# Optimization experiments

Hardware: AMD Instinct MI355X
Metric: run time of the kernel (lower is better)

The kernel has to match this reference:

```python
import jax, jax.numpy as jnp
import numpy as np

HID, HEADS = 2048, 16
Q_LORA, KV_LORA = 1536, 512
NOPE, ROPE, VD = 128, 64, 128
N_EXP, TOPK, MOE_I, SH_I = 8, 2, 1408, 2816
EPS, RSF = 1e-6, 1.0
ROPE_BASE = 10000.0


def _rms(x, w):
    return x * jax.lax.rsqrt(jnp.mean(jnp.square(x), -1, keepdims=True) + EPS) * w


def _rope(x, pos):
    # neox-style rotary on last dim; x: [T, H, d], pos: [T]
    d = x.shape[-1]
    inv = 1.0 / (ROPE_BASE ** (jnp.arange(0, d, 2, dtype=jnp.float32) / d))
    ang = pos.astype(jnp.float32)[:, None] * inv  # [T, d/2]
    cos, sin = jnp.cos(ang)[:, None, :], jnp.sin(ang)[:, None, :]
    x1, x2 = x[..., : d // 2], x[..., d // 2:]
    return jnp.concatenate([x1 * cos - x2 * sin, x2 * cos + x1 * sin], -1)


def setup_inputs() -> dict:
    key = jax.random.key(0)
    ks = jax.random.split(key, 16)
    T, s, f = 1024, 0.02, jnp.float32
    return {
        'positions': jnp.arange(T, dtype=jnp.int32),
        'hidden_states': jax.random.normal(ks[0], (T, HID), f),
        'residual': jax.random.normal(ks[1], (T, HID), f),
        'w_in_ln': jnp.ones((HID,), f),
        'w_post_ln': jnp.ones((HID,), f),
        'w_q_ln': jnp.ones((Q_LORA,), f),
        'w_kv_ln': jnp.ones((KV_LORA,), f),
        'w_qkv_a': jax.random.normal(ks[2], (HID, Q_LORA + KV_LORA + ROPE), f) * s,
        'w_q_b': jax.random.normal(ks[3], (Q_LORA, HEADS * (NOPE + ROPE)), f) * s,
        'w_kv_b': jax.random.normal(ks[4], (KV_LORA, HEADS * (NOPE + VD)), f) * s,
        'w_o': jax.random.normal(ks[5], (HEADS * VD, HID), f) * s,
        'gate_w': jax.random.normal(ks[6], (HID, N_EXP), f) * s,
        'we_gate': jax.random.normal(ks[7], (N_EXP, HID, MOE_I), f) * s,
        'we_up': jax.random.normal(ks[8], (N_EXP, HID, MOE_I), f) * s,
        'we_down': jax.random.normal(ks[9], (N_EXP, MOE_I, HID), f) * s,
        'ws_gate': jax.random.normal(ks[10], (HID, SH_I), f) * s,
        'ws_up': jax.random.normal(ks[11], (HID, SH_I), f) * s,
        'ws_down': jax.random.normal(ks[12], (SH_I, HID), f) * s,
    }


def reference(positions, hidden_states, residual, w_in_ln, w_post_ln, w_q_ln, w_kv_ln,
              w_qkv_a, w_q_b, w_kv_b, w_o, gate_w, we_gate, we_up, we_down,
              ws_gate, ws_up, ws_down):
    T = hidden_states.shape[0]
    # fused_add_rms_norm: residual <- x + residual; x <- rmsnorm(residual)
    residual = hidden_states + residual
    h = _rms(residual, w_in_ln)
    # fused qkv_a projection and split
    qkv = h @ w_qkv_a  # [T, q_lora + kv_lora + rope]
    q_c = _rms(qkv[:, :Q_LORA], w_q_ln)
    kv_c = _rms(qkv[:, Q_LORA:Q_LORA + KV_LORA], w_kv_ln)
    k_pe = qkv[:, Q_LORA + KV_LORA:][:, None, :]  # [T, 1, rope]
    # MLA up-projections
    q = (q_c @ w_q_b).reshape(T, HEADS, NOPE + ROPE)
    q_nope, q_pe = q[..., :NOPE], q[..., NOPE:]
    kv = (kv_c @ w_kv_b).reshape(T, HEADS, NOPE + VD)
    k_nope, v = kv[..., :NOPE], kv[..., NOPE:]
    q_pe = _rope(q_pe, positions)
    k_pe = _rope(k_pe, positions)
    q = jnp.concatenate([q_nope, q_pe], -1)  # [T, H, nope+rope]
    k = jnp.concatenate([k_nope, jnp.broadcast_to(k_pe, (T, HEADS, ROPE))], -1)
    scores = jnp.einsum('qhd,khd->hqk', q, k) * (NOPE + ROPE) ** -0.5
    causal = jnp.tril(jnp.ones((T, T), bool))
    scores = jnp.where(causal, scores, jnp.finfo(scores.dtype).min)
    p = jax.nn.softmax(scores, -1)
    attn_out = jnp.einsum('hqk,khd->qhd', p, v).reshape(T, HEADS * VD) @ w_o
    # post-attention fused add + norm
    residual = residual + attn_out
    h = _rms(residual, w_post_ln)
    # MoE gate: softmax scores, top-k, renormalized combine weights
    probs = jax.nn.softmax(h @ gate_w, -1)
    tw, ti = jax.lax.top_k(probs, TOPK)
    tw = tw / jnp.sum(tw, -1, keepdims=True)
    comb = jnp.sum(jax.nn.one_hot(ti, N_EXP, dtype=h.dtype) * tw[..., None], 1)  # [T, E]
    # routed experts (dense grouped-GEMM reference, SwiGLU)
    g = jnp.einsum('th,ehi->eti', h, we_gate)
    u = jnp.einsum('th,ehi->eti', h, we_up)
    y = jnp.einsum('eti,eih->eth', jax.nn.silu(g) * u, we_down)
    routed = jnp.einsum('te,eth->th', comb, y) * RSF
    # shared experts
    shared = (jax.nn.silu(h @ ws_gate) * (h @ ws_up)) @ ws_down
    return routed + shared, residual
```

## Files before the change

kernel.cpp:

```cpp
#include <hip/hip_runtime.h>
#include <hip/hip_bf16.h>

typedef unsigned short u16;
typedef __attribute__((ext_vector_type(8))) short bf16x8;
typedef __attribute__((ext_vector_type(4))) float f32x4;
typedef __attribute__((ext_vector_type(8))) unsigned short u16x8;
typedef __attribute__((ext_vector_type(4))) unsigned short u16x4;

#define T_TOK 1024
#define HID 2048
#define HEADS 16
#define Q_LORA 1536
#define KV_LORA 512
#define NOPE 128
#define ROPED 64
#define VD 128
#define N_EXP 8
#define MOE_I 1408
#define SH_I 2816
#define QKV_N 2112
#define QKV_LD 2176
#define QD 192
#define KVD 256
#define EPSF 1e-6f
#define NEG_BIG (-3.4e38f)

__device__ __forceinline__ u16 f2bf(float f) {
  union { float f; unsigned u; } x; x.f = f;
  unsigned r = x.u + 0x7fffu + ((x.u >> 16) & 1u);
  return (u16)(r >> 16);
}
__device__ __forceinline__ float bf2f(u16 h) {
  union { unsigned u; float f; } x; x.u = ((unsigned)h) << 16; return x.f;
}
__device__ __forceinline__ void split2(float f, u16& hi, u16& lo) {
  hi = f2bf(f);
  lo = f2bf(f - bf2f(hi));
}

__device__ __forceinline__ void gload16(const u16* g, const u16* l) {
  __builtin_amdgcn_global_load_lds(
      (const __attribute__((address_space(1))) void*)g,
      (__attribute__((address_space(3))) void*)l, 16, 0, 0);
}

__device__ __forceinline__ float block_sum(float v, float* s) {
  #pragma unroll
  for (int o = 32; o > 0; o >>= 1) v += __shfl_down(v, o, 64);
  int w = threadIdx.x >> 6, lane = threadIdx.x & 63;
  __syncthreads();
  if (lane == 0) s[w] = v;
  __syncthreads();
  float r = s[0];
  for (int i = 1; i < 4; ++i) r += s[i];
  return r;
}
__device__ __forceinline__ float block_max(float v, float* s) {
  #pragma unroll
  for (int o = 32; o > 0; o >>= 1) v = fmaxf(v, __shfl_down(v, o, 64));
  int w = threadIdx.x >> 6, lane = threadIdx.x & 63;
  __syncthreads();
  if (lane == 0) s[w] = v;
  __syncthreads();
  float r = s[0];
  for (int i = 1; i < 4; ++i) r = fmaxf(r, s[i]);
  return r;
}

__global__ __launch_bounds__(256) void gemm_bf16(
    const u16* __restrict__ A, long asz, int lda,
    const u16* __restrict__ B, long bsz, int ldb,
    float* __restrict__ C, u16* __restrict__ Cb, long csz, int ldc,
    const float* __restrict__ Cadd, const u16* __restrict__ CaddB, int ldcadd,
    int K, float alpha, int causal, int mode,
    float* __restrict__ pbuf, int ksplit, int stot, int soff,
    const int* __restrict__ gidx, const int* __restrict__ gcnt) {
  const int bm = blockIdx.y << 7, bn = blockIdx.x << 7;
  const int zz = blockIdx.z;
  const int z = (ksplit > 1) ? (zz / ksplit) : zz;
  const int s = (ksplit > 1) ? (zz % ksplit) : 0;
  if (gcnt && bm >= gcnt[z]) return;
  A += (long)z * asz; B += (long)z * bsz;
  if (C) C += (long)z * csz;
  if (Cb) Cb += (long)z * csz;
  if (Cadd && !pbuf) Cadd += (long)z * csz;
  if (CaddB) CaddB += (long)z * csz;
  const int tid = threadIdx.x, lane = tid & 63, wid = tid >> 6;

  if (causal && bn >= bm + 128) return;

  __shared__ alignas(16) u16 As[128 * 32];
  __shared__ alignas(16) u16 Bs[128 * 32];

  const int wr = wid >> 1, wc = wid & 1;
  f32x4 acc[4][4];
  #pragma unroll
  for (int m = 0; m < 4; ++m)
    #pragma unroll
    for (int n = 0; n < 4; ++n) acc[m][n] = f32x4{0.f, 0.f, 0.f, 0.f};

  const int srow = (wid << 5) + (lane >> 2);
  const int scol = (lane & 3) << 3;
  const int arow = (wr << 6) + (lane & 15);
  const int brow = (wc << 6) + (lane & 15);
  const int koff = (lane >> 4) << 3;

  long ga0, ga1;
  {
    int r0 = srow, r1 = srow + 16;
    if (gidx) {
      const int* tk = gidx + (long)z * T_TOK;
      ga0 = (long)tk[bm + r0]; ga1 = (long)tk[bm + r1];
    } else {
      ga0 = (long)(bm + r0); ga1 = (long)(bm + r1);
    }
  }

  const int kseg = K / ksplit;
  const int kbeg = s * kseg, kend = kbeg + kseg;

  for (int k0 = kbeg; k0 < kend; k0 += 32) {
    gload16(A + ga0 * lda + k0 + scol, &As[(wid << 10)]);
    gload16(A + ga1 * lda + k0 + scol, &As[(wid << 10) + 512]);
    gload16(B + (long)(bn + srow) * ldb + k0 + scol, &Bs[(wid << 10)]);
    gload16(B + (long)(bn + srow + 16) * ldb + k0 + scol, &Bs[(wid << 10) + 512]);
    __syncthreads();
    bf16x8 a[4], b[4];
    #pragma unroll
    for (int m = 0; m < 4; ++m) a[m] = *(const bf16x8*)&As[((arow + (m << 4)) << 5) + koff];
    #pragma unroll
    for (int n = 0; n < 4; ++n) b[n] = *(const bf16x8*)&Bs[((brow + (n << 4)) << 5) + koff];
    #pragma unroll
    for (int m = 0; m < 4; ++m)
      #pragma unroll
      for (int n = 0; n < 4; ++n)
        acc[m][n] = __builtin_amdgcn_mfma_f32_16x16x32_bf16(a[m], b[n], acc[m][n], 0, 0, 0);
    __syncthreads();
  }

  const int rbase = bm + (wr << 6) + ((lane >> 4) << 2);
  const int cbase = bn + (wc << 6) + (lane & 15);

  if (pbuf) {
    long pstride = (long)(gridDim.y << 7) * ldc;
    float* pp = pbuf + ((long)z * stot + soff + s) * pstride;
    #pragma unroll
    for (int m = 0; m < 4; ++m)
      #pragma unroll
      for (int j = 0; j < 4; ++j) {
        int r = rbase + (m << 4) + j;
        #pragma unroll
        for (int n = 0; n < 4; ++n) {
          int cc = cbase + (n << 4);
          pp[(long)r * ldc + cc] = acc[m][n][j];
        }
      }
    return;
  }

  #pragma unroll
  for (int m = 0; m < 4; ++m) {
    #pragma unroll
    for (int j = 0; j < 4; ++j) {
      int r = rbase + (m << 4) + j;
      #pragma unroll
      for (int n = 0; n < 4; ++n) {
        int cc = cbase + (n << 4);
        float v = acc[m][n][j] * alpha;
        if (mode == 0) {
          if (Cadd) v += Cadd[(long)r * ldcadd + cc];
          if (causal && cc > r) v = NEG_BIG;
          C[(long)r * ldc + cc] = v;
        } else if (mode == 1) {
          float gg = Cadd[(long)r * ldcadd + cc];
          float sgv = gg / (1.f + expf(-gg));
          Cb[(long)r * ldc + cc] = f2bf(sgv * v);
        } else if (mode == 2) {
          Cb[(long)r * ldc + cc] = f2bf(v);
        } else {
          float gg = bf2f(CaddB[(long)r * ldcadd + cc]);
          float sgv = gg / (1.f + expf(-gg));
          Cb[(long)r * ldc + cc] = f2bf(sgv * v);
        }
      }
    }
  }
}

__global__ __launch_bounds__(256) void reduce_sk(
    const float* __restrict__ pbuf, long pstride, int S,
    float* __restrict__ C, u16* __restrict__ Cb, long csz, int ldc, int Nc,
    const float* __restrict__ Cadd, long caddsz, int ldcadd,
    float alpha, int mode) {
  const int z = blockIdx.y;
  const float* pz = pbuf + (long)z * S * pstride;
  long idx = ((long)blockIdx.x * 256 + threadIdx.x) * 8;
  long r = idx / Nc; int c = (int)(idx - r * Nc);
  float a[8] = {0.f, 0.f, 0.f, 0.f, 0.f, 0.f, 0.f, 0.f};
  for (int s = 0; s < S; ++s) {
    const float* pp = pz + (long)s * pstride + idx;
    float4 x = *(const float4*)pp;
    float4 y = *(const float4*)(pp + 4);
    a[0] += x.x; a[1] += x.y; a[2] += x.z; a[3] += x.w;
    a[4] += y.x; a[5] += y.y; a[6] += y.z; a[7] += y.w;
  }
  long ob = (long)z * csz + r * ldc + c;
  if (mode == 0) {
    #pragma unroll
    for (int k = 0; k < 8; ++k) {
      float v = a[k] * alpha;
      if (Cadd) v += Cadd[(long)z * caddsz + r * ldcadd + c + k];
      C[ob + k] = v;
    }
  } else {
    u16x8 o;
    #pragma unroll
    for (int k = 0; k < 8; ++k) {
      float gg = Cadd[(long)z * caddsz + r * ldcadd + c + k];
      float sgv = gg / (1.f + expf(-gg));
      o[k] = f2bf(sgv * a[k] * alpha);
    }
    *(u16x8*)&Cb[ob] = o;
  }
}

__global__ __launch_bounds__(256) void transpose_f32_bf16(
    const float* __restrict__ src, long sbs, int ld_src, int Cvalid,
    u16* __restrict__ dst, long dbs, int ld_dst) {
  __shared__ float tile[64][65];
  src += (long)blockIdx.z * sbs; dst += (long)blockIdx.z * dbs;
  const int c0 = blockIdx.x << 6, r0 = blockIdx.y << 6;
  const int tid = threadIdx.x;
  const int tc = (tid & 15) << 2, tr0 = tid >> 4;
  const bool valid = c0 < Cvalid;
  #pragma unroll
  for (int i = 0; i < 4; ++i) {
    int r = tr0 + (i << 4);
    float4 v;
    if (valid) v = *(const float4*)&src[(long)(r0 + r) * ld_src + c0 + tc];
    else { v.x = 0.f; v.y = 0.f; v.z = 0.f; v.w = 0.f; }
    tile[r][tc] = v.x; tile[r][tc + 1] = v.y; tile[r][tc + 2] = v.z; tile[r][tc + 3] = v.w;
  }
  __syncthreads();
  const int oc = tid >> 2, seg = tid & 3;
  u16x8 o0, o1;
  #pragma unroll
  for (int k = 0; k < 8; ++k) o0[k] = f2bf(tile[(seg << 4) + k][oc]);
  #pragma unroll
  for (int k = 0; k < 8; ++k) o1[k] = f2bf(tile[(seg << 4) + 8 + k][oc]);
  u16* dp = &dst[(long)(c0 + oc) * ld_dst + r0 + (seg << 4)];
  *(u16x8*)dp = o0;
  *(u16x8*)(dp + 8) = o1;
}

__global__ __launch_bounds__(256) void transpose_split3(
    const float* __restrict__ src, long sbs, int ld_src, int Cvalid,
    u16* __restrict__ dst, long dbs, int Kp) {
  __shared__ float tile[64][65];
  src += (long)blockIdx.z * sbs; dst += (long)blockIdx.z * dbs;
  const int c0 = blockIdx.x << 6, r0 = blockIdx.y << 6;
  const int tid = threadIdx.x;
  const int tc = (tid & 15) << 2, tr0 = tid >> 4;
  const bool valid = c0 < Cvalid;
  #pragma unroll
  for (int i = 0; i < 4; ++i) {
    int r = tr0 + (i << 4);
    float4 v;
    if (valid) v = *(const float4*)&src[(long)(r0 + r) * ld_src + c0 + tc];
    else { v.x = 0.f; v.y = 0.f; v.z = 0.f; v.w = 0.f; }
    tile[r][tc] = v.x; tile[r][tc + 1] = v.y; tile[r][tc + 2] = v.z; tile[r][tc + 3] = v.w;
  }
  __syncthreads();
  const int oc = tid >> 2, seg = tid & 3;
  u16x8 h0, h1, l0, l1;
  #pragma unroll
  for (int k = 0; k < 8; ++k) {
    u16 hi, lo; split2(tile[(seg << 4) + k][oc], hi, lo);
    h0[k] = hi; l0[k] = lo;
  }
  #pragma unroll
  for (int k = 0; k < 8; ++k) {
    u16 hi, lo; split2(tile[(seg << 4) + 8 + k][oc], hi, lo);
    h1[k] = hi; l1[k] = lo;
  }
  const int ldd = 3 * Kp;
  u16* dp = &dst[(long)(c0 + oc) * ldd + r0 + (seg << 4)];
  *(u16x8*)dp = h0;            *(u16x8*)(dp + 8) = h1;
  *(u16x8*)(dp + Kp) = h0;     *(u16x8*)(dp + Kp + 8) = h1;
  *(u16x8*)(dp + 2 * Kp) = l0; *(u16x8*)(dp + 2 * Kp + 8) = l1;
}

__global__ __launch_bounds__(256) void conv_split3_kernel(
    const float* __restrict__ src, u16* __restrict__ dst, int C, long n) {
  long stride = (long)gridDim.x * 2048;
  for (long i = ((long)blockIdx.x * 256 + threadIdx.x) * 8; i < n; i += stride) {
    long r = i / C; int c = (int)(i - r * C);
    float4 a = *(const float4*)&src[i];
    float4 b = *(const float4*)&src[i + 4];
    u16x8 hv, lv;
    u16 hi, lo;
    split2(a.x, hi, lo); hv[0] = hi; lv[0] = lo;
    split2(a.y, hi, lo); hv[1] = hi; lv[1] = lo;
    split2(a.z, hi, lo); hv[2] = hi; lv[2] = lo;
    split2(a.w, hi, lo); hv[3] = hi; lv[3] = lo;
    split2(b.x, hi, lo); hv[4] = hi; lv[4] = lo;
    split2(b.y, hi, lo); hv[5] = hi; lv[5] = lo;
    split2(b.z, hi, lo); hv[6] = hi; lv[6] = lo;
    split2(b.w, hi, lo); hv[7] = hi; lv[7] = lo;
    u16* base = dst + r * (long)(3 * C) + c;
    *(u16x8*)base = hv;
    *(u16x8*)(base + C) = lv;
    *(u16x8*)(base + 2 * C) = hv;
  }
}

__global__ __launch_bounds__(256) void add_rms_kernel(
    const float* __restrict__ hs, const float* __restrict__ res,
    const float* __restrict__ w, float* __restrict__ resid1, u16* __restrict__ h3) {
  __shared__ float sbuf[4];
  int t = blockIdx.x;
  float v[8]; float ss = 0.f;
  #pragma unroll
  for (int i = 0; i < 8; ++i) {
    int j = threadIdx.x + (i << 8);
    float x = hs[(long)t * HID + j] + res[(long)t * HID + j];
    v[i] = x; resid1[(long)t * HID + j] = x; ss += x * x;
  }
  ss = block_sum(ss, sbuf);
  float sc = rsqrtf(ss / (float)HID + EPSF);
  u16* base = h3 + (long)t * (3 * HID);
  #pragma unroll
  for (int i = 0; i < 8; ++i) {
    int j = threadIdx.x + (i << 8);
    u16 hi, lo; split2(v[i] * sc * w[j], hi, lo);
    base[j] = hi; base[HID + j] = lo; base[2 * HID + j] = hi;
  }
}

template <int NW, bool SPLIT, bool WF32>
__global__ __launch_bounds__(256) void rms_rows_kernel(
    const float* __restrict__ in, int ldin, const float* __restrict__ w,
    u16* __restrict__ outb, float* __restrict__ outf) {
  __shared__ float sbuf[4];
  int t = blockIdx.x;
  const int W = NW * 256;
  float v[NW]; float ss = 0.f;
  #pragma unroll
  for (int i = 0; i < NW; ++i) {
    int j = threadIdx.x + (i << 8);
    float x = in[(long)t * ldin + j];
    v[i] = x; ss += x * x;
  }
  ss = block_sum(ss, sbuf);
  float sc = rsqrtf(ss / (float)W + EPSF);
  #pragma unroll
  for (int i = 0; i < NW; ++i) {
    int j = threadIdx.x + (i << 8);
    float y = v[i] * sc * w[j];
    if (SPLIT) {
      u16 hi, lo; split2(y, hi, lo);
      u16* base = outb + (long)t * (3 * W);
      base[j] = hi; base[W + j] = lo; base[2 * W + j] = hi;
    } else {
      outb[(long)t * W + j] = f2bf(y);
    }
    if (WF32) outf[(long)t * W + j] = y;
  }
}

__global__ __launch_bounds__(256) void rope_kernel(
    const int* __restrict__ pos, float* __restrict__ q,
    const float* __restrict__ qkv, float* __restrict__ kpe) {
  int t = blockIdx.x;
  float fp = (float)pos[t];
  for (int item = threadIdx.x; item < 544; item += 256) {
    int i = item & 31;
    float inv = expf(-((float)i * (2.f / 64.f)) * 9.210340371976184f);
    float ang = fp * inv;
    float c = cosf(ang), s = sinf(ang);
    if (item < 512) {
      int hh = item >> 5;
      long base = (long)t * (HEADS * QD) + hh * QD + NOPE;
      float x1 = q[base + i], x2 = q[base + 32 + i];
      q[base + i] = x1 * c - x2 * s;
      q[base + 32 + i] = x2 * c + x1 * s;
    } else {
      long base = (long)t * QKV_LD + (Q_LORA + KV_LORA);
      float x1 = qkv[base + i], x2 = qkv[base + 32 + i];
      kpe[(long)t * 64 + i] = x1 * c - x2 * s;
      kpe[(long)t * 64 + 32 + i] = x2 * c + x1 * s;
    }
  }
}

__global__ __launch_bounds__(192) void build_q3_kernel(
    const float* __restrict__ qbuf, u16* __restrict__ q3) {
  int t = blockIdx.x, h = blockIdx.y, d = threadIdx.x;
  float x = qbuf[(long)t * (HEADS * QD) + h * QD + d];
  u16 hi, lo; split2(x, hi, lo);
  u16* base = q3 + ((long)h * T_TOK + t) * (3 * QD);
  base[d] = hi; base[QD + d] = lo; base[2 * QD + d] = hi;
}

__global__ __launch_bounds__(192) void build_kmat3_kernel(
    const float* __restrict__ kv, const float* __restrict__ kpe,
    u16* __restrict__ kmat3) {
  int t = blockIdx.x, h = blockIdx.y, d = threadIdx.x;
  float v = (d < NOPE) ? kv[(long)t * (HEADS * KVD) + h * KVD + d]
                       : kpe[(long)t * 64 + (d - NOPE)];
  u16 hi, lo; split2(v, hi, lo);
  u16* base = kmat3 + ((long)h * T_TOK + t) * (3 * QD);
  base[d] = hi; base[QD + d] = hi; base[2 * QD + d] = lo;
}

__global__ __launch_bounds__(256) void softmax_kernel(
    const float* __restrict__ S, u16* __restrict__ P2) {
  __shared__ float sbuf[4];
  long row = blockIdx.x;
  int r = (int)(row & (T_TOK - 1));
  const float* p = S + row * T_TOK;
  float4 v = ((const float4*)p)[threadIdx.x];
  int c0 = threadIdx.x << 2;
  if (c0 + 0 > r) v.x = NEG_BIG;
  if (c0 + 1 > r) v.y = NEG_BIG;
  if (c0 + 2 > r) v.z = NEG_BIG;
  if (c0 + 3 > r) v.w = NEG_BIG;
  float m = fmaxf(fmaxf(v.x, v.y), fmaxf(v.z, v.w));
  m = block_max(m, sbuf);
  v.x = expf(v.x - m); v.y = expf(v.y - m); v.z = expf(v.z - m); v.w = expf(v.w - m);
  float s = v.x + v.y + v.z + v.w;
  s = block_sum(s, sbuf);
  float inv = 1.f / s;
  u16x4 hv, lv;
  u16 hi, lo;
  split2(v.x * inv, hi, lo); hv[0] = hi; lv[0] = lo;
  split2(v.y * inv, hi, lo); hv[1] = hi; lv[1] = lo;
  split2(v.z * inv, hi, lo); hv[2] = hi; lv[2] = lo;
  split2(v.w * inv, hi, lo); hv[3] = hi; lv[3] = lo;
  u16* base = P2 + row * (2 * T_TOK) + (threadIdx.x << 2);
  *(u16x4*)base = hv;
  *(u16x4*)(base + T_TOK) = lv;
}

__global__ __launch_bounds__(256) void gate_topk_kernel(
    const float* __restrict__ h2, const float* __restrict__ gw,
    int* __restrict__ ti, float* __restrict__ tw) {
  __shared__ float sbuf[4];
  __shared__ float lg[N_EXP];
  int t = blockIdx.x;
  float p[N_EXP] = {0.f, 0.f, 0.f, 0.f, 0.f, 0.f, 0.f, 0.f};
  for (int j = threadIdx.x; j < HID; j += 256) {
    float x = h2[(long)t * HID + j];
    const float* gr = gw + (long)j * N_EXP;
    #pragma unroll
    for (int e = 0; e < N_EXP; ++e) p[e] += x * gr[e];
  }
  #pragma unroll
  for (int e = 0; e < N_EXP; ++e) {
    float s = block_sum(p[e], sbuf);
    if (threadIdx.x == 0) lg[e] = s;
  }
  __syncthreads();
  if (threadIdx.x == 0) {
    float m = lg[0];
    for (int e = 1; e < N_EXP; ++e) m = fmaxf(m, lg[e]);
    float pe[N_EXP]; float s = 0.f;
    for (int e = 0; e < N_EXP; ++e) { pe[e] = expf(lg[e] - m); s += pe[e]; }
    for (int e = 0; e < N_EXP; ++e) pe[e] /= s;
    int i0 = 0;
    for (int e = 1; e < N_EXP; ++e) if (pe[e] > pe[i0]) i0 = e;
    int i1 = -1;
    for (int e = 0; e < N_EXP; ++e) if (e != i0 && (i1 < 0 || pe[e] > pe[i1])) i1 = e;
    float ssum = pe[i0] + pe[i1];
    ti[2 * t] = i0; ti[2 * t + 1] = i1;
    tw[2 * t] = pe[i0] / ssum; tw[2 * t + 1] = pe[i1] / ssum;
  }
}

__global__ __launch_bounds__(64) void route_build_kernel(
    const int* __restrict__ ti, int* __restrict__ tokidx,
    int* __restrict__ pos, int* __restrict__ cnt) {
  int e = blockIdx.x;
  int lane = threadIdx.x;
  if (e >= N_EXP) {
    for (int p = lane; p < T_TOK; p += 64) tokidx[(long)e * T_TOK + p] = p;
    if (lane == 0) cnt[e] = T_TOK;
    return;
  }
  int c = 0;
  for (int base = 0; base < T_TOK; base += 64) {
    int t = base + lane;
    int e0 = ti[2 * t], e1 = ti[2 * t + 1];
    bool match = (e0 == e) || (e1 == e);
    unsigned long long mask = __ballot(match);
    int pref = __popcll(mask & ((1ull << lane) - 1ull));
    if (match) {
      int p = c + pref;
      tokidx[(long)e * T_TOK + p] = t;
      pos[2 * t + ((e0 == e) ? 0 : 1)] = p;
    }
    c += __popcll(mask);
  }
  for (int p = c + lane; p < T_TOK; p += 64) tokidx[(long)e * T_TOK + p] = 0;
  if (lane == 0) cnt[e] = c;
}

__global__ __launch_bounds__(256) void combine_out_kernel(
    const u16* __restrict__ y, const int* __restrict__ ti,
    const float* __restrict__ tw, const int* __restrict__ pos,
    float* __restrict__ out0) {
  int t = blockIdx.x;
  int j = threadIdx.x << 3;
  int e0 = ti[2 * t], e1 = ti[2 * t + 1];
  int p0 = pos[2 * t], p1 = pos[2 * t + 1];
  float w0 = tw[2 * t], w1 = tw[2 * t + 1];
  u16x8 a = *(const u16x8*)&y[((long)e0 * T_TOK + p0) * HID + j];
  u16x8 b = *(const u16x8*)&y[((long)e1 * T_TOK + p1) * HID + j];
  u16x8 c = *(const u16x8*)&y[((long)8 * T_TOK + t) * HID + j];
  u16x8 d = *(const u16x8*)&y[((long)9 * T_TOK + t) * HID + j];
  float* rp = out0 + (long)t * HID + j;
  #pragma unroll
  for (int k = 0; k < 8; ++k)
    rp[k] = w0 * bf2f(a[k]) + w1 * bf2f(b[k]) + bf2f(c[k]) + bf2f(d[k]);
}

extern "C" void kernel_launch(void* const* d_in, const int* in_sizes, int n_in,
                              void* d_out, int out_size, void* d_ws, size_t ws_size,
                              hipStream_t stream) {
  (void)in_sizes; (void)n_in; (void)out_size; (void)ws_size;
  const int*   positions = (const int*)d_in[0];
  const float* hs        = (const float*)d_in[1];
  const float* res       = (const float*)d_in[2];
  const float* w_in_ln   = (const float*)d_in[3];
  const float* w_post_ln = (const float*)d_in[4];
  const float* w_q_ln    = (const float*)d_in[5];
  const float* w_kv_ln   = (const float*)d_in[6];
  const float* w_qkv_a   = (const float*)d_in[7];
  const float* w_q_b     = (const float*)d_in[8];
  const float* w_kv_b    = (const float*)d_in[9];
  const float* w_o       = (const float*)d_in[10];
  const float* gate_w    = (const float*)d_in[11];
  const float* we_gate   = (const float*)d_in[12];
  const float* we_up     = (const float*)d_in[13];
  const float* we_down   = (const float*)d_in[14];
  const float* ws_gate   = (const float*)d_in[15];
  const float* ws_up     = (const float*)d_in[16];
  const float* ws_dn     = (const float*)d_in[17];

  float* out0   = (float*)d_out;
  float* resid2 = out0 + (long)T_TOK * HID;

  char* Wb = (char*)d_ws;
  size_t off = 0;
  #define CARVE(name, type, bytes) type* name = (type*)(Wb + off); off += (((size_t)(bytes) + 255) & ~(size_t)255)

  CARVE(wqkvaT3, u16, (size_t)QKV_LD * 3 * HID * 2);
  CARVE(wqbT3,   u16, (size_t)(HEADS * QD) * 3 * Q_LORA * 2);
  CARVE(wkvbT3,  u16, (size_t)(HEADS * KVD) * 3 * KV_LORA * 2);
  CARVE(woT3,    u16, (size_t)HID * 3 * HID * 2);

  size_t pool = off;
  CARVE(resid1, float, (size_t)T_TOK * HID * 4);
  CARVE(h3,     u16,   (size_t)T_TOK * 3 * HID * 2);
  CARVE(qkv,    float, (size_t)T_TOK * QKV_LD * 4);
  CARVE(qc3,    u16,   (size_t)T_TOK * 3 * Q_LORA * 2);
  CARVE(kvc3,   u16,   (size_t)T_TOK * 3 * KV_LORA * 2);
  CARVE(qbuf,   float, (size_t)T_TOK * HEADS * QD * 4);
  CARVE(q3,     u16,   (size_t)HEADS * T_TOK * 3 * QD * 2);
  CARVE(kvbuf,  float, (size_t)T_TOK * HEADS * KVD * 4);
  CARVE(kpe,    float, (size_t)T_TOK * 64 * 4);
  CARVE(kmat3,  u16,   (size_t)HEADS * T_TOK * 3 * QD * 2);
  CARVE(vt3,    u16,   (size_t)HEADS * VD * 3 * T_TOK * 2);
  CARVE(scores, float, (size_t)HEADS * T_TOK * T_TOK * 4);
  CARVE(P2,     u16,   (size_t)HEADS * T_TOK * 2 * T_TOK * 2);
  CARVE(attn,   float, (size_t)T_TOK * HID * 4);
  CARVE(attn3,  u16,   (size_t)T_TOK * 3 * HID * 2);
  size_t endA = off;
  float* pbufA = scores;

  off = pool;
  CARVE(wegT10, u16, (size_t)10 * MOE_I * HID * 2);
  CARVE(weuT10, u16, (size_t)10 * MOE_I * HID * 2);
  CARVE(wedT10, u16, (size_t)10 * HID * MOE_I * 2);
  CARVE(h2,     float, (size_t)T_TOK * HID * 4);
  CARVE(h2_b,   u16,   (size_t)T_TOK * HID * 2);
  CARVE(ti,     int,   (size_t)T_TOK * 2 * 4);
  CARVE(tw,     float, (size_t)T_TOK * 2 * 4);
  CARVE(pos,    int,   (size_t)T_TOK * 2 * 4);
  CARVE(tokidx, int,   (size_t)10 * T_TOK * 4);
  CARVE(cnt,    int,   64);
  CARVE(gact_g, u16,   (size_t)10 * T_TOK * MOE_I * 2);
  CARVE(gact,   u16,   (size_t)10 * T_TOK * MOE_I * 2);
  CARVE(ycomp,  u16,   (size_t)10 * T_TOK * HID * 2);
  if (off < endA) off = endA;
  #undef CARVE

  const float* nullf = nullptr;
  float* nullC = nullptr;
  u16* nullB = nullptr;
  const u16* nullBB = nullptr;
  const int* nullI = nullptr;

  hipLaunchKernelGGL(transpose_split3, dim3(QKV_LD / 64, HID / 64, 1), dim3(256), 0, stream,
                     w_qkv_a, 0L, QKV_N, QKV_N, wqkvaT3, 0L, HID);
  hipLaunchKernelGGL(transpose_split3, dim3(HEADS * QD / 64, Q_LORA / 64, 1), dim3(256), 0, stream,
                     w_q_b, 0L, HEADS * QD, HEADS * QD, wqbT3, 0L, Q_LORA);
  hipLaunchKernelGGL(transpose_split3, dim3(HEADS * KVD / 64, KV_LORA / 64, 1), dim3(256), 0, stream,
                     w_kv_b, 0L, HEADS * KVD, HEADS * KVD, wkvbT3, 0L, KV_LORA);
  hipLaunchKernelGGL(transpose_split3, dim3(HID / 64, HID / 64, 1), dim3(256), 0, stream,
                     w_o, 0L, HID, HID, woT3, 0L, HID);

  hipLaunchKernelGGL(add_rms_kernel, dim3(T_TOK), dim3(256), 0, stream,
                     hs, res, w_in_ln, resid1, h3);
  hipLaunchKernelGGL(gemm_bf16, dim3(QKV_LD / 128, T_TOK / 128, 4), dim3(256), 0, stream,
                     h3, 0L, 3 * HID, wqkvaT3, 0L, 3 * HID,
                     nullC, nullB, 0L, QKV_LD, nullf, nullBB, 0, 3 * HID, 1.f, 0, 0,
                     pbufA, 4, 4, 0, nullI, nullI);
  hipLaunchKernelGGL(reduce_sk, dim3(T_TOK * QKV_LD / 2048, 1), dim3(256), 0, stream,
                     pbufA, (long)T_TOK * QKV_LD, 4,
                     qkv, nullB, 0L, QKV_LD, QKV_LD, nullf, 0L, 0, 1.f, 0);
  hipLaunchKernelGGL((rms_rows_kernel<6, true, false>), dim3(T_TOK), dim3(256), 0, stream,
                     qkv, QKV_LD, w_q_ln, qc3, (float*)nullptr);
  hipLaunchKernelGGL((rms_rows_kernel<2, true, false>), dim3(T_TOK), dim3(256), 0, stream,
                     qkv + Q_LORA, QKV_LD, w_kv_ln, kvc3, (float*)nullptr);
  hipLaunchKernelGGL(gemm_bf16, dim3(HEADS * QD / 128, T_TOK / 128, 4), dim3(256), 0, stream,
                     qc3, 0L, 3 * Q_LORA, wqbT3, 0L, 3 * Q_LORA,
                     nullC, nullB, 0L, HEADS * QD, nullf, nullBB, 0, 3 * Q_LORA, 1.f, 0, 0,
                     pbufA, 4, 4, 0, nullI, nullI);
  hipLaunchKernelGGL(reduce_sk, dim3(T_TOK * HEADS * QD / 2048, 1), dim3(256), 0, stream,
                     pbufA, (long)T_TOK * HEADS * QD, 4,
                     qbuf, nullB, 0L, HEADS * QD, HEADS * QD, nullf, 0L, 0, 1.f, 0);
  hipLaunchKernelGGL(gemm_bf16, dim3(HEADS * KVD / 128, T_TOK / 128, 4), dim3(256), 0, stream,
                     kvc3, 0L, 3 * KV_LORA, wkvbT3, 0L, 3 * KV_LORA,
                     nullC, nullB, 0L, HEADS * KVD, nullf, nullBB, 0, 3 * KV_LORA, 1.f, 0, 0,
                     pbufA, 4, 4, 0, nullI, nullI);
  hipLaunchKernelGGL(reduce_sk, dim3(T_TOK * HEADS * KVD / 2048, 1), dim3(256), 0, stream,
                     pbufA, (long)T_TOK * HEADS * KVD, 4,
                     kvbuf, nullB, 0L, HEADS * KVD, HEADS * KVD, nullf, 0L, 0, 1.f, 0);
  hipLaunchKernelGGL(rope_kernel, dim3(T_TOK), dim3(256), 0, stream,
                     positions, qbuf, qkv, kpe);
  hipLaunchKernelGGL(build_q3_kernel, dim3(T_TOK, HEADS), dim3(192), 0, stream, qbuf, q3);
  hipLaunchKernelGGL(build_kmat3_kernel, dim3(T_TOK, HEADS), dim3(192), 0, stream,
                     kvbuf, kpe, kmat3);
  hipLaunchKernelGGL(transpose_split3, dim3(VD / 64, T_TOK / 64, HEADS), dim3(256), 0, stream,
                     kvbuf + NOPE, 256L, HEADS * KVD, VD, vt3, (long)VD * 3 * T_TOK, T_TOK);
  hipLaunchKernelGGL(gemm_bf16, dim3(T_TOK / 128, T_TOK / 128, HEADS), dim3(256), 0, stream,
                     q3, (long)T_TOK * 3 * QD, 3 * QD,
                     kmat3, (long)T_TOK * 3 * QD, 3 * QD,
                     scores, nullB, (long)T_TOK * T_TOK, T_TOK,
                     nullf, nullBB, 0, 576, 0.07216878364870322f, 1, 0,
                     nullC, 1, 1, 0, nullI, nullI);
  hipLaunchKernelGGL(softmax_kernel, dim3(HEADS * T_TOK), dim3(256), 0, stream, scores, P2);
  hipLaunchKernelGGL(gemm_bf16, dim3(VD / 128, T_TOK / 128, HEADS * 4), dim3(256), 0, stream,
                     P2, (long)T_TOK * 2 * T_TOK, 2 * T_TOK,
                     vt3, (long)VD * 3 * T_TOK, 3 * T_TOK,
                     nullC, nullB, 0L, VD, nullf, nullBB, 0, 2 * T_TOK, 1.f, 0, 0,
                     pbufA, 4, 6, 0, nullI, nullI);
  hipLaunchKernelGGL(gemm_bf16, dim3(VD / 128, T_TOK / 128, HEADS * 2), dim3(256), 0, stream,
                     P2, (long)T_TOK * 2 * T_TOK, 2 * T_TOK,
                     vt3 + 2 * T_TOK, (long)VD * 3 * T_TOK, 3 * T_TOK,
                     nullC, nullB, 0L, VD, nullf, nullBB, 0, T_TOK, 1.f, 0, 0,
                     pbufA, 2, 6, 4, nullI, nullI);
  hipLaunchKernelGGL(reduce_sk, dim3(T_TOK * VD / 2048, HEADS), dim3(256), 0, stream,
                     pbufA, (long)T_TOK * VD, 6,
                     attn, nullB, (long)VD, HID, VD, nullf, 0L, 0, 1.f, 0);
  hipLaunchKernelGGL(conv_split3_kernel, dim3(1024), dim3(256), 0, stream,
                     attn, attn3, HID, (long)T_TOK * HID);
  hipLaunchKernelGGL(gemm_bf16, dim3(HID / 128, T_TOK / 128, 4), dim3(256), 0, stream,
                     attn3, 0L, 3 * HID, woT3, 0L, 3 * HID,
                     nullC, nullB, 0L, HID, nullf, nullBB, 0, 3 * HID, 1.f, 0, 0,
                     pbufA, 4, 4, 0, nullI, nullI);
  hipLaunchKernelGGL(reduce_sk, dim3(T_TOK * HID / 2048, 1), dim3(256), 0, stream,
                     pbufA, (long)T_TOK * HID, 4,
                     resid2, nullB, 0L, HID, HID, resid1, 0L, HID, 1.f, 0);

  hipLaunchKernelGGL(transpose_f32_bf16, dim3(MOE_I / 64, HID / 64, N_EXP), dim3(256), 0, stream,
                     we_gate, (long)HID * MOE_I, MOE_I, MOE_I, wegT10, (long)MOE_I * HID, HID);
  hipLaunchKernelGGL(transpose_f32_bf16, dim3(MOE_I / 64, HID / 64, 2), dim3(256), 0, stream,
                     ws_gate, (long)MOE_I, SH_I, MOE_I,
                     wegT10 + (size_t)8 * MOE_I * HID, (long)MOE_I * HID, HID);
  hipLaunchKernelGGL(transpose_f32_bf16, dim3(MOE_I / 64, HID / 64, N_EXP), dim3(256), 0, stream,
                     we_up, (long)HID * MOE_I, MOE_I, MOE_I, weuT10, (long)MOE_I * HID, HID);
  hipLaunchKernelGGL(transpose_f32_bf16, dim3(MOE_I / 64, HID / 64, 2), dim3(256), 0, stream,
                     ws_up, (long)MOE_I, SH_I, MOE_I,
                     weuT10 + (size_t)8 * MOE_I * HID, (long)MOE_I * HID, HID);
  hipLaunchKernelGGL(transpose_f32_bf16, dim3(HID / 64, MOE_I / 64, N_EXP), dim3(256), 0, stream,
                     we_down, (long)MOE_I * HID, HID, HID, wedT10, (long)HID * MOE_I, MOE_I);
  hipLaunchKernelGGL(transpose_f32_bf16, dim3(HID / 64, MOE_I / 64, 2), dim3(256), 0, stream,
                     ws_dn, (long)MOE_I * HID, HID, HID,
                     wedT10 + (size_t)8 * HID * MOE_I, (long)HID * MOE_I, MOE_I);

  hipLaunchKernelGGL((rms_rows_kernel<8, false, true>), dim3(T_TOK), dim3(256), 0, stream,
                     resid2, HID, w_post_ln, h2_b, h2);
  hipLaunchKernelGGL(gate_topk_kernel, dim3(T_TOK), dim3(256), 0, stream,
                     h2, gate_w, ti, tw);
  hipLaunchKernelGGL(route_build_kernel, dim3(10), dim3(64), 0, stream,
                     ti, tokidx, pos, cnt);
  hipLaunchKernelGGL(gemm_bf16, dim3(MOE_I / 128, T_TOK / 128, 10), dim3(256), 0, stream,
                     h2_b, 0L, HID, wegT10, (long)MOE_I * HID, HID,
                     nullC, gact_g, (long)T_TOK * MOE_I, MOE_I,
                     nullf, nullBB, 0, HID, 1.f, 0, 2, nullC, 1, 1, 0, tokidx, cnt);
  hipLaunchKernelGGL(gemm_bf16, dim3(MOE_I / 128, T_TOK / 128, 10), dim3(256), 0, stream,
                     h2_b, 0L, HID, weuT10, (long)MOE_I * HID, HID,
                     nullC, gact, (long)T_TOK * MOE_I, MOE_I,
                     nullf, gact_g, MOE_I, HID, 1.f, 0, 3, nullC, 1, 1, 0, tokidx, cnt);
  hipLaunchKernelGGL(gemm_bf16, dim3(HID / 128, T_TOK / 128, 10), dim3(256), 0, stream,
                     gact, (long)T_TOK * MOE_I, MOE_I,
                     wedT10, (long)HID * MOE_I, MOE_I,
                     nullC, ycomp, (long)T_TOK * HID, HID,
                     nullf, nullBB, 0, MOE_I, 1.f, 0, 2, nullC, 1, 1, 0, nullI, cnt);
  hipLaunchKernelGGL(combine_out_kernel, dim3(T_TOK), dim3(256), 0, stream,
                     ycomp, ti, tw, pos, out0);
}
```

Baseline: 914.3 us.

## Fuse MoE gate/up GEMMs into one wide GEMM and add XCD-aware block remap

```diff
diff --git a/kernel.cpp b/kernel.cpp
--- a/kernel.cpp
+++ b/kernel.cpp
@@ -44,6 +44,17 @@
       (__attribute__((address_space(3))) void*)l, 16, 0, 0);
 }
 
+__device__ __forceinline__ void xcd_unswizzle(int& bx, int& by, int& bz) {
+  int gx = gridDim.x, gy = gridDim.y;
+  int nwg = gx * gy * gridDim.z;
+  int flat = blockIdx.x + gx * (blockIdx.y + gy * blockIdx.z);
+  int q8 = nwg >> 3, r8 = nwg & 7;
+  int xcd = flat & 7, pos = flat >> 3;
+  int wg = (xcd < r8 ? xcd * (q8 + 1) : r8 * (q8 + 1) + (xcd - r8) * q8) + pos;
+  bx = wg % gx; int tmp = wg / gx;
+  by = tmp % gy; bz = tmp / gy;
+}
+
 __device__ __forceinline__ float block_sum(float v, float* s) {
   #pragma unroll
   for (int o = 32; o > 0; o >>= 1) v += __shfl_down(v, o, 64);
@@ -71,12 +82,17 @@
     const u16* __restrict__ A, long asz, int lda,
     const u16* __restrict__ B, long bsz, int ldb,
     float* __restrict__ C, u16* __restrict__ Cb, long csz, int ldc,
-    const float* __restrict__ Cadd, const u16* __restrict__ CaddB, int ldcadd,
+    const float* __restrict__ Cadd, int ldcadd,
     int K, float alpha, int causal, int mode,
     float* __restrict__ pbuf, int ksplit, int stot, int soff,
-    const int* __restrict__ gidx, const int* __restrict__ gcnt) {
-  const int bm = blockIdx.y << 7, bn = blockIdx.x << 7;
-  const int zz = blockIdx.z;
+    const int* __restrict__ gidx, const int* __restrict__ gcnt, int swz) {
+  int bxi, byi, zz;
+  if (swz) {
+    xcd_unswizzle(bxi, byi, zz);
+  } else {
+    bxi = blockIdx.x; byi = blockIdx.y; zz = blockIdx.z;
+  }
+  const int bm = byi << 7, bn = bxi << 7;
   const int z = (ksplit > 1) ? (zz / ksplit) : zz;
   const int s = (ksplit > 1) ? (zz % ksplit) : 0;
   if (gcnt && bm >= gcnt[z]) return;
@@ -84,7 +100,6 @@
   if (C) C += (long)z * csz;
   if (Cb) Cb += (long)z * csz;
   if (Cadd && !pbuf) Cadd += (long)z * csz;
-  if (CaddB) CaddB += (long)z * csz;
   const int tid = threadIdx.x, lane = tid & 63, wid = tid >> 6;
 
   if (causal && bn >= bm + 128) return;
@@ -107,12 +122,11 @@
 
   long ga0, ga1;
   {
-    int r0 = srow, r1 = srow + 16;
     if (gidx) {
       const int* tk = gidx + (long)z * T_TOK;
-      ga0 = (long)tk[bm + r0]; ga1 = (long)tk[bm + r1];
+      ga0 = (long)tk[bm + srow]; ga1 = (long)tk[bm + srow + 16];
     } else {
-      ga0 = (long)(bm + r0); ga1 = (long)(bm + r1);
+      ga0 = (long)(bm + srow); ga1 = (long)(bm + srow + 16);
     }
   }
 
@@ -175,12 +189,8 @@
           float gg = Cadd[(long)r * ldcadd + cc];
           float sgv = gg / (1.f + expf(-gg));
           Cb[(long)r * ldc + cc] = f2bf(sgv * v);
-        } else if (mode == 2) {
+        } else {
           Cb[(long)r * ldc + cc] = f2bf(v);
-        } else {
-          float gg = bf2f(CaddB[(long)r * ldcadd + cc]);
-          float sgv = gg / (1.f + expf(-gg));
-          Cb[(long)r * ldc + cc] = f2bf(sgv * v);
         }
       }
     }
@@ -505,6 +515,26 @@
   if (lane == 0) cnt[e] = c;
 }
 
+__global__ __launch_bounds__(256) void silu_mul_moe_kernel(
+    const u16* __restrict__ gug, const int* __restrict__ cnt,
+    u16* __restrict__ gact) {
+  int r = blockIdx.x, e = blockIdx.y;
+  int padded = (cnt[e] + 127) & ~127;
+  if (r >= padded) return;
+  int j = threadIdx.x << 3;
+  if (j >= MOE_I) return;
+  const u16* src = gug + ((long)e * T_TOK + r) * (2 * MOE_I) + j;
+  u16x8 gv = *(const u16x8*)src;
+  u16x8 uv = *(const u16x8*)(src + MOE_I);
+  u16x8 o;
+  #pragma unroll
+  for (int k = 0; k < 8; ++k) {
+    float g = bf2f(gv[k]);
+    o[k] = f2bf(g / (1.f + expf(-g)) * bf2f(uv[k]));
+  }
+  *(u16x8*)&gact[((long)e * T_TOK + r) * MOE_I + j] = o;
+}
+
 __global__ __launch_bounds__(256) void combine_out_kernel(
     const u16* __restrict__ y, const int* __restrict__ ti,
     const float* __restrict__ tw, const int* __restrict__ pos,
@@ -579,8 +609,7 @@
   float* pbufA = scores;
 
   off = pool;
-  CARVE(wegT10, u16, (size_t)10 * MOE_I * HID * 2);
-  CARVE(weuT10, u16, (size_t)10 * MOE_I * HID * 2);
+  CARVE(wegu,   u16, (size_t)10 * (2 * MOE_I) * HID * 2);
   CARVE(wedT10, u16, (size_t)10 * HID * MOE_I * 2);
   CARVE(h2,     float, (size_t)T_TOK * HID * 4);
   CARVE(h2_b,   u16,   (size_t)T_TOK * HID * 2);
@@ -589,7 +618,7 @@
   CARVE(pos,    int,   (size_t)T_TOK * 2 * 4);
   CARVE(tokidx, int,   (size_t)10 * T_TOK * 4);
   CARVE(cnt,    int,   64);
-  CARVE(gact_g, u16,   (size_t)10 * T_TOK * MOE_I * 2);
+  CARVE(gug,    u16,   (size_t)10 * T_TOK * (2 * MOE_I) * 2);
   CARVE(gact,   u16,   (size_t)10 * T_TOK * MOE_I * 2);
   CARVE(ycomp,  u16,   (size_t)10 * T_TOK * HID * 2);
   if (off < endA) off = endA;
@@ -598,7 +627,6 @@
   const float* nullf = nullptr;
   float* nullC = nullptr;
   u16* nullB = nullptr;
-  const u16* nullBB = nullptr;
   const int* nullI = nullptr;
 
   hipLaunchKernelGGL(transpose_split3, dim3(QKV_LD / 64, HID / 64, 1), dim3(256), 0, stream,
@@ -614,8 +642,8 @@
                      hs, res, w_in_ln, resid1, h3);
   hipLaunchKernelGGL(gemm_bf16, dim3(QKV_LD / 128, T_TOK / 128, 4), dim3(256), 0, stream,
                      h3, 0L, 3 * HID, wqkvaT3, 0L, 3 * HID,
-                     nullC, nullB, 0L, QKV_LD, nullf, nullBB, 0, 3 * HID, 1.f, 0, 0,
-                     pbufA, 4, 4, 0, nullI, nullI);
+                     nullC, nullB, 0L, QKV_LD, nullf, 0, 3 * HID, 1.f, 0, 0,
+                     pbufA, 4, 4, 0, nullI, nullI, 0);
   hipLaunchKernelGGL(reduce_sk, dim3(T_TOK * QKV_LD / 2048, 1), dim3(256), 0, stream,
                      pbufA, (long)T_TOK * QKV_LD, 4,
                      qkv, nullB, 0L, QKV_LD, QKV_LD, nullf, 0L, 0, 1.f, 0);
@@ -625,15 +653,15 @@
                      qkv + Q_LORA, QKV_LD, w_kv_ln, kvc3, (float*)nullptr);
   hipLaunchKernelGGL(gemm_bf16, dim3(HEADS * QD / 128, T_TOK / 128, 4), dim3(256), 0, stream,
                      qc3, 0L, 3 * Q_LORA, wqbT3, 0L, 3 * Q_LORA,
-                     nullC, nullB, 0L, HEADS * QD, nullf, nullBB, 0, 3 * Q_LORA, 1.f, 0, 0,
-                     pbufA, 4, 4, 0, nullI, nullI);
+                     nullC, nullB, 0L, HEADS * QD, nullf, 0, 3 * Q_LORA, 1.f, 0, 0,
+                     pbufA, 4, 4, 0, nullI, nullI, 0);
   hipLaunchKernelGGL(reduce_sk, dim3(T_TOK * HEADS * QD / 2048, 1), dim3(256), 0, stream,
                      pbufA, (long)T_TOK * HEADS * QD, 4,
                      qbuf, nullB, 0L, HEADS * QD, HEADS * QD, nullf, 0L, 0, 1.f, 0);
   hipLaunchKernelGGL(gemm_bf16, dim3(HEADS * KVD / 128, T_TOK / 128, 4), dim3(256), 0, stream,
                      kvc3, 0L, 3 * KV_LORA, wkvbT3, 0L, 3 * KV_LORA,
-                     nullC, nullB, 0L, HEADS * KVD, nullf, nullBB, 0, 3 * KV_LORA, 1.f, 0, 0,
-                     pbufA, 4, 4, 0, nullI, nullI);
+                     nullC, nullB, 0L, HEADS * KVD, nullf, 0, 3 * KV_LORA, 1.f, 0, 0,
+                     pbufA, 4, 4, 0, nullI, nullI, 0);
   hipLaunchKernelGGL(reduce_sk, dim3(T_TOK * HEADS * KVD / 2048, 1), dim3(256), 0, stream,
                      pbufA, (long)T_TOK * HEADS * KVD, 4,
                      kvbuf, nullB, 0L, HEADS * KVD, HEADS * KVD, nullf, 0L, 0, 1.f, 0);
@@ -648,19 +676,19 @@
                      q3, (long)T_TOK * 3 * QD, 3 * QD,
                      kmat3, (long)T_TOK * 3 * QD, 3 * QD,
                      scores, nullB, (long)T_TOK * T_TOK, T_TOK,
-                     nullf, nullBB, 0, 576, 0.07216878364870322f, 1, 0,
-                     nullC, 1, 1, 0, nullI, nullI);
+                     nullf, 0, 576, 0.07216878364870322f, 1, 0,
+                     nullC, 1, 1, 0, nullI, nullI, 0);
   hipLaunchKernelGGL(softmax_kernel, dim3(HEADS * T_TOK), dim3(256), 0, stream, scores, P2);
   hipLaunchKernelGGL(gemm_bf16, dim3(VD / 128, T_TOK / 128, HEADS * 4), dim3(256), 0, stream,
                      P2, (long)T_TOK * 2 * T_TOK, 2 * T_TOK,
                      vt3, (long)VD * 3 * T_TOK, 3 * T_TOK,
-                     nullC, nullB, 0L, VD, nullf, nullBB, 0, 2 * T_TOK, 1.f, 0, 0,
-                     pbufA, 4, 6, 0, nullI, nullI);
+                     nullC, nullB, 0L, VD, nullf, 0, 2 * T_TOK, 1.f, 0, 0,
+                     pbufA, 4, 6, 0, nullI, nullI, 0);
   hipLaunchKernelGGL(gemm_bf16, dim3(VD / 128, T_TOK / 128, HEADS * 2), dim3(256), 0, stream,
                      P2, (long)T_TOK * 2 * T_TOK, 2 * T_TOK,
                      vt3 + 2 * T_TOK, (long)VD * 3 * T_TOK, 3 * T_TOK,
-                     nullC, nullB, 0L, VD, nullf, nullBB, 0, T_TOK, 1.f, 0, 0,
-                     pbufA, 2, 6, 4, nullI, nullI);
+                     nullC, nullB, 0L, VD, nullf, 0, T_TOK, 1.f, 0, 0,
+                     pbufA, 2, 6, 4, nullI, nullI, 0);
   hipLaunchKernelGGL(reduce_sk, dim3(T_TOK * VD / 2048, HEADS), dim3(256), 0, stream,
                      pbufA, (long)T_TOK * VD, 6,
                      attn, nullB, (long)VD, HID, VD, nullf, 0L, 0, 1.f, 0);
@@ -668,22 +696,25 @@
                      attn, attn3, HID, (long)T_TOK * HID);
   hipLaunchKernelGGL(gemm_bf16, dim3(HID / 128, T_TOK / 128, 4), dim3(256), 0, stream,
                      attn3, 0L, 3 * HID, woT3, 0L, 3 * HID,
-                     nullC, nullB, 0L, HID, nullf, nullBB, 0, 3 * HID, 1.f, 0, 0,
-                     pbufA, 4, 4, 0, nullI, nullI);
+                     nullC, nullB, 0L, HID, nullf, 0, 3 * HID, 1.f, 0, 0,
+                     pbufA, 4, 4, 0, nullI, nullI, 0);
   hipLaunchKernelGGL(reduce_sk, dim3(T_TOK * HID / 2048, 1), dim3(256), 0, stream,
                      pbufA, (long)T_TOK * HID, 4,
                      resid2, nullB, 0L, HID, HID, resid1, 0L, HID, 1.f, 0);
 
   hipLaunchKernelGGL(transpose_f32_bf16, dim3(MOE_I / 64, HID / 64, N_EXP), dim3(256), 0, stream,
-                     we_gate, (long)HID * MOE_I, MOE_I, MOE_I, wegT10, (long)MOE_I * HID, HID);
+                     we_gate, (long)HID * MOE_I, MOE_I, MOE_I,
+                     wegu, (long)(2 * MOE_I) * HID, HID);
+  hipLaunchKernelGGL(transpose_f32_bf16, dim3(MOE_I / 64, HID / 64, N_EXP), dim3(256), 0, stream,
+                     we_up, (long)HID * MOE_I, MOE_I, MOE_I,
+                     wegu + (size_t)MOE_I * HID, (long)(2 * MOE_I) * HID, HID);
   hipLaunchKernelGGL(transpose_f32_bf16, dim3(MOE_I / 64, HID / 64, 2), dim3(256), 0, stream,
                      ws_gate, (long)MOE_I, SH_I, MOE_I,
-                     wegT10 + (size_t)8 * MOE_I * HID, (long)MOE_I * HID, HID);
-  hipLaunchKernelGGL(transpose_f32_bf16, dim3(MOE_I / 64, HID / 64, N_EXP), dim3(256), 0, stream,
-                     we_up, (long)HID * MOE_I, MOE_I, MOE_I, weuT10, (long)MOE_I * HID, HID);
+                     wegu + (size_t)8 * (2 * MOE_I) * HID, (long)(2 * MOE_I) * HID, HID);
   hipLaunchKernelGGL(transpose_f32_bf16, dim3(MOE_I / 64, HID / 64, 2), dim3(256), 0, stream,
                      ws_up, (long)MOE_I, SH_I, MOE_I,
-                     weuT10 + (size_t)8 * MOE_I * HID, (long)MOE_I * HID, HID);
+                     wegu + (size_t)8 * (2 * MOE_I) * HID + (size_t)MOE_I * HID,
+                     (long)(2 * MOE_I) * HID, HID);
   hipLaunchKernelGGL(transpose_f32_bf16, dim3(HID / 64, MOE_I / 64, N_EXP), dim3(256), 0, stream,
                      we_down, (long)MOE_I * HID, HID, HID, wedT10, (long)HID * MOE_I, MOE_I);
   hipLaunchKernelGGL(transpose_f32_bf16, dim3(HID / 64, MOE_I / 64, 2), dim3(256), 0, stream,
@@ -696,19 +727,17 @@
                      h2, gate_w, ti, tw);
   hipLaunchKernelGGL(route_build_kernel, dim3(10), dim3(64), 0, stream,
                      ti, tokidx, pos, cnt);
-  hipLaunchKernelGGL(gemm_bf16, dim3(MOE_I / 128, T_TOK / 128, 10), dim3(256), 0, stream,
-                     h2_b, 0L, HID, wegT10, (long)MOE_I * HID, HID,
-                     nullC, gact_g, (long)T_TOK * MOE_I, MOE_I,
-                     nullf, nullBB, 0, HID, 1.f, 0, 2, nullC, 1, 1, 0, tokidx, cnt);
-  hipLaunchKernelGGL(gemm_bf16, dim3(MOE_I / 128, T_TOK / 128, 10), dim3(256), 0, stream,
-                     h2_b, 0L, HID, weuT10, (long)MOE_I * HID, HID,
-                     nullC, gact, (long)T_TOK * MOE_I, MOE_I,
-                     nullf, gact_g, MOE_I, HID, 1.f, 0, 3, nullC, 1, 1, 0, tokidx, cnt);
+  hipLaunchKernelGGL(gemm_bf16, dim3(2 * MOE_I / 128, T_TOK / 128, 10), dim3(256), 0, stream,
+                     h2_b, 0L, HID, wegu, (long)(2 * MOE_I) * HID, HID,
+                     nullC, gug, (long)T_TOK * (2 * MOE_I), 2 * MOE_I,
+                     nullf, 0, HID, 1.f, 0, 2, nullC, 1, 1, 0, tokidx, cnt, 1);
+  hipLaunchKernelGGL(silu_mul_moe_kernel, dim3(T_TOK, 10), dim3(256), 0, stream,
+                     gug, cnt, gact);
   hipLaunchKernelGGL(gemm_bf16, dim3(HID / 128, T_TOK / 128, 10), dim3(256), 0, stream,
                      gact, (long)T_TOK * MOE_I, MOE_I,
                      wedT10, (long)HID * MOE_I, MOE_I,
                      nullC, ycomp, (long)T_TOK * HID, HID,
-                     nullf, nullBB, 0, MOE_I, 1.f, 0, 2, nullC, 1, 1, 0, nullI, cnt);
+                     nullf, 0, MOE_I, 1.f, 0, 2, nullC, 1, 1, 0, nullI, cnt, 1);
   hipLaunchKernelGGL(combine_out_kernel, dim3(T_TOK), dim3(256), 0, stream,
                      ycomp, ti, tw, pos, out0);
 }
```

Measured after the change: 931.1 us. About the same (+1.8%).
